# Kernel optimization log

Measured on AMD Instinct MI355X. Metric: run time of the kernel, lower is better.

## Reference

```python
import jax, jax.numpy as jnp
import numpy as np

NUM_QUANTS = 256
RES_CH = 120
SKIP_CH = 240
K = 2
NUM_BLOCKS = 16
CYCLE = 8
DILATIONS = [2 ** (i % CYCLE) for i in range(NUM_BLOCKS)]


def causal_conv1d(x, w, b, dilation=1):
    # x: [B, Cin, T], w: [Cout, Cin, K], left-pad for causality
    pad = (w.shape[-1] - 1) * dilation
    y = jax.lax.conv_general_dilated(
        x, w, window_strides=(1,), padding=[(pad, 0)],
        rhs_dilation=(dilation,), dimension_numbers=('NCH', 'OIH', 'NCH'))
    return y + b[None, :, None]


def setup_inputs() -> dict:
    key = jax.random.key(0)
    ks = jax.random.split(key, 16)
    B, T = 8, 16384
    s = 0.1
    inp = {
        'waveforms': jax.random.normal(ks[0], (B, T), jnp.float32),
        'W_in': jax.random.normal(ks[1], (RES_CH, 1, 1), jnp.float32) * s,
        'b_in': jnp.zeros((RES_CH,), jnp.float32),
        'Wf': jax.random.normal(ks[2], (NUM_BLOCKS, RES_CH, RES_CH, K), jnp.float32) * s,
        'bf': jnp.zeros((NUM_BLOCKS, RES_CH), jnp.float32),
        'Wg': jax.random.normal(ks[3], (NUM_BLOCKS, RES_CH, RES_CH, K), jnp.float32) * s,
        'bg': jnp.zeros((NUM_BLOCKS, RES_CH), jnp.float32),
        'Wres': jax.random.normal(ks[4], (NUM_BLOCKS, RES_CH, RES_CH, 1), jnp.float32) * s,
        'bres': jnp.zeros((NUM_BLOCKS, RES_CH), jnp.float32),
        'Wskip': jax.random.normal(ks[5], (NUM_BLOCKS, SKIP_CH, RES_CH, 1), jnp.float32) * s,
        'bskip': jnp.zeros((NUM_BLOCKS, SKIP_CH), jnp.float32),
        'W1': jax.random.normal(ks[6], (NUM_QUANTS, SKIP_CH, 1), jnp.float32) * s,
        'b1': jnp.zeros((NUM_QUANTS,), jnp.float32),
        'W2': jax.random.normal(ks[7], (NUM_QUANTS, NUM_QUANTS, 1), jnp.float32) * s,
        'b2': jnp.zeros((NUM_QUANTS,), jnp.float32),
    }
    return inp


def reference(waveforms, W_in, b_in, Wf, bf, Wg, bg, Wres, bres, Wskip, bskip, W1, b1, W2, b2):
    # input 1x1 conv: [B, T] -> [B, RES_CH, T]
    x = causal_conv1d(waveforms[:, None, :], W_in, b_in)
    skip_sum = jnp.zeros((x.shape[0], SKIP_CH, x.shape[2]), x.dtype)
    for i in range(NUM_BLOCKS):
        d = DILATIONS[i]
        f = jnp.tanh(causal_conv1d(x, Wf[i], bf[i], d))
        g = jax.nn.sigmoid(causal_conv1d(x, Wg[i], bg[i], d))
        z = f * g  # gated activation
        skip_sum = skip_sum + causal_conv1d(z, Wskip[i], bskip[i])
        x = x + causal_conv1d(z, Wres[i], bres[i])
    h = jax.nn.relu(skip_sum)
    h = jax.nn.relu(causal_conv1d(h, W1, b1))
    logits = causal_conv1d(h, W2, b2)  # [B, NUM_QUANTS, T]
    return logits
```

## Files before the change

kernel.cpp:

```cpp
#include <hip/hip_runtime.h>
#include <cstddef>

#define TT 16384
#define NBATCH 8
#define CH 128
#define RES 120
#define SKIPC 240
#define NQ 256
#define NT2 32
#define NTF 64
#define KZ 2048

typedef __attribute__((ext_vector_type(8))) short bf8;
typedef __attribute__((ext_vector_type(4))) short s4;
typedef __attribute__((ext_vector_type(4))) float f32x4;

__device__ __forceinline__ short f2bf(float f) {
  unsigned u = __builtin_bit_cast(unsigned, f);
  u += 0x7fffu + ((u >> 16) & 1u);
  return (short)(u >> 16);
}
__device__ __forceinline__ float bf2f(short s) {
  unsigned u = ((unsigned)(unsigned short)s) << 16;
  return __builtin_bit_cast(float, u);
}

__global__ void k_pack(const float* __restrict__ Wf, const float* __restrict__ Wg,
                       const float* __restrict__ Wres, const float* __restrict__ Wskip,
                       const float* __restrict__ W1, const float* __restrict__ W2,
                       const float* __restrict__ bf, const float* __restrict__ bg,
                       const float* __restrict__ bres, const float* __restrict__ bskip,
                       short* __restrict__ Afg, short* __restrict__ Ars,
                       short* __restrict__ W1p, short* __restrict__ W2p,
                       float* __restrict__ biasp,
                       short* __restrict__ Wskp, float* __restrict__ bsum, int do2) {
  const int NAFG = 16 * 256 * 256;
  const int NARS = 16 * 384 * 128;
  const int NW = 256 * 256;
  const int NBIA = 16 * (128 * 3 + 256);
  const int NWSK = 256 * 2048;
  const int total = NAFG + NARS + 2 * NW + NBIA + NWSK + 256;
  for (int idx = blockIdx.x * blockDim.x + threadIdx.x; idx < total;
       idx += gridDim.x * blockDim.x) {
    if (idx < NAFG) {
      int i = idx >> 16, rem = idx & 65535, m = rem >> 8, k = rem & 255;
      int tap = k >> 7, ci = k & 127;
      float v = 0.f;
      if (ci < 120) {
        if (m < 120) v = Wf[((i * 120 + m) * 120 + ci) * 2 + tap];
        else if (m >= 128 && m < 248) v = Wg[((i * 120 + (m - 128)) * 120 + ci) * 2 + tap];
      }
      Afg[idx] = f2bf(v);
    } else if (idx < NAFG + NARS) {
      int j = idx - NAFG;
      int i = j / 49152, rem = j % 49152, m = rem >> 7, k = rem & 127;
      float v = 0.f;
      if (k < 120) {
        if (m < 120) v = Wres[(i * 120 + m) * 120 + k];
        else if (m >= 128 && m < 368) v = Wskip[(i * 240 + (m - 128)) * 120 + k];
      }
      Ars[j] = f2bf(v);
    } else if (idx < NAFG + NARS + NW) {
      int j = idx - NAFG - NARS, q = j >> 8, k = j & 255;
      W1p[j] = f2bf(k < 240 ? W1[q * 240 + k] : 0.f);
    } else if (idx < NAFG + NARS + 2 * NW) {
      int j = idx - NAFG - NARS - NW;
      W2p[j] = f2bf(W2[j]);
    } else if (idx < NAFG + NARS + 2 * NW + NBIA) {
      int j = idx - NAFG - NARS - 2 * NW;
      float v = 0.f;
      if (j < 2048) { int i = j >> 7, c = j & 127; if (c < 120) v = bf[i * 120 + c]; }
      else if (j < 4096) { int jj = j - 2048; int i = jj >> 7, c = jj & 127; if (c < 120) v = bg[i * 120 + c]; }
      else if (j < 6144) { int jj = j - 4096; int i = jj >> 7, c = jj & 127; if (c < 120) v = bres[i * 120 + c]; }
      else { int jj = j - 6144; int i = jj >> 8, c = jj & 255; if (c < 240) v = bskip[i * 240 + c]; }
      biasp[j] = v;
    } else if (idx < NAFG + NARS + 2 * NW + NBIA + NWSK) {
      if (do2) {
        int j = idx - NAFG - NARS - 2 * NW - NBIA;
        int m = j >> 11, k = j & 2047;
        int layer = k >> 7, ci = k & 127;
        float v = 0.f;
        if (m < 240 && ci < 120) v = Wskip[((size_t)layer * 240 + m) * 120 + ci];
        Wskp[j] = f2bf(v);
      }
    } else {
      if (do2) {
        int m = idx - (NAFG + NARS + 2 * NW + NBIA + NWSK);
        float v = 0.f;
        if (m < 240)
          for (int l = 0; l < 16; l++) v += bskip[l * 240 + m];
        bsum[m] = v;
      }
    }
  }
}

__global__ void k_input(const float* __restrict__ wave, const float* __restrict__ win,
                        const float* __restrict__ bin, short* __restrict__ x0) {
  int idx = blockIdx.x * blockDim.x + threadIdx.x;
  if (idx >= NBATCH * TT) return;
  float wv = wave[idx];
  short* row = x0 + (size_t)idx * CH;
  for (int c = 0; c < CH; c += 4) {
    s4 v;
#pragma unroll
    for (int j = 0; j < 4; j++)
      v[j] = (c + j < 120) ? f2bf(win[c + j] * wv + bin[c + j]) : (short)0;
    *(s4*)(row + c) = v;
  }
}

__global__ __launch_bounds__(256) void k_res2(
    const short* __restrict__ xin, short* __restrict__ xout,
    short* __restrict__ zg,
    const short* __restrict__ Afg, const short* __restrict__ Ars,
    const float* __restrict__ biasp, int layer, int dil, int b_off) {
  __shared__ short xc[NT2][136];
  __shared__ short xd[NT2][136];
  __shared__ short zT[NT2][136];
  const int bl = blockIdx.y;
  const int b = b_off + bl;
  const int t0 = blockIdx.x * NT2;
  const int tid = threadIdx.x;
  const int lane = tid & 63, w = tid >> 6;
  const int l15 = lane & 15, l4 = lane >> 4;
  const size_t xbase = (size_t)b * TT * CH;

#pragma unroll
  for (int j = 0; j < 2; j++) {
    int i = tid + j * 256;
    int t = i >> 4, c8 = i & 15;
    *(bf8*)&xc[t][c8 * 8] = *(const bf8*)(xin + xbase + (size_t)(t0 + t) * CH + c8 * 8);
    int ts = t0 + t - dil;
    bf8 vd = (bf8)(short)0;
    if (ts >= 0) vd = *(const bf8*)(xin + xbase + (size_t)ts * CH + c8 * 8);
    *(bf8*)&xd[t][c8 * 8] = vd;
  }
  __syncthreads();

  f32x4 fa[2][2], ga[2][2];
#pragma unroll
  for (int i = 0; i < 2; i++)
#pragma unroll
    for (int j = 0; j < 2; j++) { fa[i][j] = (f32x4)0.f; ga[i][j] = (f32x4)0.f; }
  const short* pAf[2];
  const short* pAg[2];
#pragma unroll
  for (int mt = 0; mt < 2; mt++) {
    pAf[mt] = Afg + (size_t)(w * 32 + mt * 16 + l15) * 256 + l4 * 8;
    pAg[mt] = Afg + (size_t)(128 + w * 32 + mt * 16 + l15) * 256 + l4 * 8;
  }
#pragma unroll
  for (int kk = 0; kk < 8; kk++) {
    const int k = kk * 32;
    bf8 Bv[2];
#pragma unroll
    for (int nt = 0; nt < 2; nt++)
      Bv[nt] = (kk < 4) ? *(const bf8*)&xd[nt * 16 + l15][k + l4 * 8]
                        : *(const bf8*)&xc[nt * 16 + l15][(k - 128) + l4 * 8];
#pragma unroll
    for (int mt = 0; mt < 2; mt++) {
      bf8 Av = *(const bf8*)(pAf[mt] + k);
      bf8 Gv = *(const bf8*)(pAg[mt] + k);
#pragma unroll
      for (int nt = 0; nt < 2; nt++) {
        fa[mt][nt] = __builtin_amdgcn_mfma_f32_16x16x32_bf16(Av, Bv[nt], fa[mt][nt], 0, 0, 0);
        ga[mt][nt] = __builtin_amdgcn_mfma_f32_16x16x32_bf16(Gv, Bv[nt], ga[mt][nt], 0, 0, 0);
      }
    }
  }

  const float* bf_ = biasp + (size_t)layer * 128;
  const float* bg_ = biasp + 2048 + (size_t)layer * 128;
#pragma unroll
  for (int mt = 0; mt < 2; mt++) {
    const int mb = w * 32 + mt * 16 + l4 * 4;
#pragma unroll
    for (int nt = 0; nt < 2; nt++) {
      s4 zp;
#pragma unroll
      for (int r = 0; r < 4; r++) {
        float f = fa[mt][nt][r] + bf_[mb + r];
        float g = ga[mt][nt][r] + bg_[mb + r];
        float th = 1.f - 2.f / (__expf(2.f * f) + 1.f);
        float sg = 1.f / (1.f + __expf(-g));
        zp[r] = f2bf(th * sg);
      }
      *(s4*)&zT[nt * 16 + l15][mb] = zp;
    }
  }
  __syncthreads();

#pragma unroll
  for (int j = 0; j < 2; j++) {
    int i = tid + j * 256;
    int t = i >> 4, c8 = i & 15;
    bf8 v = *(const bf8*)&zT[t][c8 * 8];
    __builtin_nontemporal_store(
        v, (bf8*)(zg + ((size_t)(bl * TT + t0 + t) * 16 + layer) * 128 + c8 * 8));
  }

  f32x4 acc[2][2];
#pragma unroll
  for (int i = 0; i < 2; i++)
#pragma unroll
    for (int j = 0; j < 2; j++) acc[i][j] = (f32x4)0.f;
  const short* pA[2];
#pragma unroll
  for (int mt = 0; mt < 2; mt++)
    pA[mt] = Ars + (size_t)(w * 32 + mt * 16 + l15) * 128 + l4 * 8;
#pragma unroll
  for (int kk = 0; kk < 4; kk++) {
    const int k = kk * 32;
    bf8 Bv[2];
#pragma unroll
    for (int nt = 0; nt < 2; nt++) Bv[nt] = *(const bf8*)&zT[nt * 16 + l15][k + l4 * 8];
#pragma unroll
    for (int mt = 0; mt < 2; mt++) {
      bf8 Av = *(const bf8*)(pA[mt] + k);
#pragma unroll
      for (int nt = 0; nt < 2; nt++)
        acc[mt][nt] = __builtin_amdgcn_mfma_f32_16x16x32_bf16(Av, Bv[nt], acc[mt][nt], 0, 0, 0);
    }
  }

  const float* br_ = biasp + 4096 + (size_t)layer * 128;
#pragma unroll
  for (int mt = 0; mt < 2; mt++) {
    const int m = w * 32 + mt * 16 + l4 * 4;
#pragma unroll
    for (int nt = 0; nt < 2; nt++) {
      int t = t0 + nt * 16 + l15;
      s4 xv = *(const s4*)&xc[nt * 16 + l15][m];
      s4 ov;
#pragma unroll
      for (int r = 0; r < 4; r++)
        ov[r] = f2bf(bf2f(xv[r]) + acc[mt][nt][r] + br_[m + r]);
      *(s4*)(xout + xbase + (size_t)t * CH + m) = ov;
    }
  }
}

__global__ __launch_bounds__(256) void k_head2(
    const short* __restrict__ zg, const short* __restrict__ Wskp,
    const float* __restrict__ bsum,
    const short* __restrict__ W1p, const float* __restrict__ b1,
    const short* __restrict__ W2p, const float* __restrict__ b2,
    float* __restrict__ out, int b_off) {
  __shared__ short bufA[NT2][264];
  __shared__ short bufB[NT2][264];
  const int bl = blockIdx.y;
  const int b = b_off + bl;
  const int t0 = blockIdx.x * NT2;
  const int tid = threadIdx.x;
  const int lane = tid & 63, w = tid >> 6;
  const int l15 = lane & 15, l4 = lane >> 4;

  f32x4 acc[4][2];
#pragma unroll
  for (int i = 0; i < 4; i++)
#pragma unroll
    for (int j = 0; j < 2; j++) acc[i][j] = (f32x4)0.f;

  const short* zrow = zg + (size_t)(bl * TT + t0) * KZ;

#pragma unroll
  for (int j = 0; j < 4; j++) {
    int i = tid + j * 256;
    int t = i >> 5, c8 = i & 31;
    *(bf8*)&bufA[t][c8 * 8] = *(const bf8*)(zrow + (size_t)t * KZ + c8 * 8);
  }
  __syncthreads();
  for (int c = 0; c < 8; c++) {
    short (*cur)[264] = (c & 1) ? bufB : bufA;
    short (*nxt)[264] = (c & 1) ? bufA : bufB;
    if (c < 7) {
#pragma unroll
      for (int j = 0; j < 4; j++) {
        int i = tid + j * 256;
        int t = i >> 5, c8 = i & 31;
        *(bf8*)&nxt[t][c8 * 8] =
            *(const bf8*)(zrow + (size_t)t * KZ + (c + 1) * 256 + c8 * 8);
      }
    }
#pragma unroll
    for (int kk = 0; kk < 8; kk++) {
      const int k = kk * 32;
      bf8 Bv[2];
#pragma unroll
      for (int nt = 0; nt < 2; nt++)
        Bv[nt] = *(const bf8*)&cur[nt * 16 + l15][k + l4 * 8];
#pragma unroll
      for (int mt = 0; mt < 4; mt++) {
        bf8 Av = *(const bf8*)(Wskp + (size_t)(w * 64 + mt * 16 + l15) * KZ +
                               c * 256 + k + l4 * 8);
#pragma unroll
        for (int nt = 0; nt < 2; nt++)
          acc[mt][nt] = __builtin_amdgcn_mfma_f32_16x16x32_bf16(Av, Bv[nt], acc[mt][nt], 0, 0, 0);
      }
    }
    __syncthreads();
  }

#pragma unroll
  for (int mt = 0; mt < 4; mt++) {
    const int mb = w * 64 + mt * 16 + l4 * 4;
#pragma unroll
    for (int nt = 0; nt < 2; nt++) {
      s4 hp;
#pragma unroll
      for (int r = 0; r < 4; r++)
        hp[r] = f2bf(fmaxf(acc[mt][nt][r] + bsum[mb + r], 0.f));
      *(s4*)&bufA[nt * 16 + l15][mb] = hp;
    }
  }
  __syncthreads();

#pragma unroll
  for (int i = 0; i < 4; i++)
#pragma unroll
    for (int j = 0; j < 2; j++) acc[i][j] = (f32x4)0.f;
#pragma unroll
  for (int kk = 0; kk < 8; kk++) {
    const int k = kk * 32;
    bf8 Bv[2];
#pragma unroll
    for (int nt = 0; nt < 2; nt++) Bv[nt] = *(const bf8*)&bufA[nt * 16 + l15][k + l4 * 8];
#pragma unroll
    for (int mt = 0; mt < 4; mt++) {
      bf8 Av = *(const bf8*)(W1p + (size_t)(w * 64 + mt * 16 + l15) * 256 + k + l4 * 8);
#pragma unroll
      for (int nt = 0; nt < 2; nt++)
        acc[mt][nt] = __builtin_amdgcn_mfma_f32_16x16x32_bf16(Av, Bv[nt], acc[mt][nt], 0, 0, 0);
    }
  }
#pragma unroll
  for (int mt = 0; mt < 4; mt++) {
    const int mb = w * 64 + mt * 16 + l4 * 4;
#pragma unroll
    for (int nt = 0; nt < 2; nt++) {
      s4 hp;
#pragma unroll
      for (int r = 0; r < 4; r++)
        hp[r] = f2bf(fmaxf(acc[mt][nt][r] + b1[mb + r], 0.f));
      *(s4*)&bufB[nt * 16 + l15][mb] = hp;
    }
  }
  __syncthreads();

#pragma unroll
  for (int i = 0; i < 4; i++)
#pragma unroll
    for (int j = 0; j < 2; j++) acc[i][j] = (f32x4)0.f;
#pragma unroll
  for (int kk = 0; kk < 8; kk++) {
    const int k = kk * 32;
    bf8 Bv[2];
#pragma unroll
    for (int nt = 0; nt < 2; nt++) Bv[nt] = *(const bf8*)&bufB[nt * 16 + l15][k + l4 * 8];
#pragma unroll
    for (int mt = 0; mt < 4; mt++) {
      bf8 Av = *(const bf8*)(W2p + (size_t)(w * 64 + mt * 16 + l15) * 256 + k + l4 * 8);
#pragma unroll
      for (int nt = 0; nt < 2; nt++)
        acc[mt][nt] = __builtin_amdgcn_mfma_f32_16x16x32_bf16(Av, Bv[nt], acc[mt][nt], 0, 0, 0);
    }
  }
#pragma unroll
  for (int mt = 0; mt < 4; mt++) {
    const int q = w * 64 + mt * 16 + l4 * 4;
#pragma unroll
    for (int nt = 0; nt < 2; nt++) {
      int t = t0 + nt * 16 + l15;
#pragma unroll
      for (int r = 0; r < 4; r++) {
        float v = acc[mt][nt][r] + b2[q + r];
        __builtin_nontemporal_store(v, out + ((size_t)b * NQ + q + r) * TT + t);
      }
    }
  }
}

__global__ __launch_bounds__(256) void k_res_mfma(
    const short* __restrict__ xin, short* __restrict__ xout,
    float* __restrict__ skip,
    const short* __restrict__ Afg, const short* __restrict__ Ars,
    const float* __restrict__ biasp, int layer, int dil, int first) {
  __shared__ short zT[NTF][136];
  const int b = blockIdx.y;
  const int t0 = blockIdx.x * NTF;
  const int tid = threadIdx.x;
  const int lane = tid & 63, w = tid >> 6;
  const int l15 = lane & 15, l4 = lane >> 4;
  const size_t xbase = (size_t)b * TT * CH;

  f32x4 fa[2][4], ga[2][4];
#pragma unroll
  for (int i = 0; i < 2; i++)
#pragma unroll
    for (int j = 0; j < 4; j++) { fa[i][j] = (f32x4)0.f; ga[i][j] = (f32x4)0.f; }

  const short* pBd[4];
  const short* pBc[4];
  bool vld[4];
#pragma unroll
  for (int nt = 0; nt < 4; nt++) {
    int t = t0 + nt * 16 + l15;
    int ts = t - dil;
    vld[nt] = (ts >= 0);
    pBd[nt] = xin + xbase + (size_t)(vld[nt] ? ts : 0) * CH + l4 * 8;
    pBc[nt] = xin + xbase + (size_t)t * CH + l4 * 8;
  }
  const short* pAf[2];
  const short* pAg[2];
#pragma unroll
  for (int mt = 0; mt < 2; mt++) {
    pAf[mt] = Afg + (size_t)(w * 32 + mt * 16 + l15) * 256 + l4 * 8;
    pAg[mt] = Afg + (size_t)(128 + w * 32 + mt * 16 + l15) * 256 + l4 * 8;
  }
  const bf8 zv = (bf8)(short)0;
#pragma unroll
  for (int kk = 0; kk < 8; kk++) {
    const int k = kk * 32;
    bf8 Bv[4];
#pragma unroll
    for (int nt = 0; nt < 4; nt++) {
      if (kk < 4) {
        bf8 v = *(const bf8*)(pBd[nt] + k);
        Bv[nt] = vld[nt] ? v : zv;
      } else {
        Bv[nt] = *(const bf8*)(pBc[nt] + (k - 128));
      }
    }
#pragma unroll
    for (int mt = 0; mt < 2; mt++) {
      bf8 Av = *(const bf8*)(pAf[mt] + k);
      bf8 Gv = *(const bf8*)(pAg[mt] + k);
#pragma unroll
      for (int nt = 0; nt < 4; nt++) {
        fa[mt][nt] = __builtin_amdgcn_mfma_f32_16x16x32_bf16(Av, Bv[nt], fa[mt][nt], 0, 0, 0);
        ga[mt][nt] = __builtin_amdgcn_mfma_f32_16x16x32_bf16(Gv, Bv[nt], ga[mt][nt], 0, 0, 0);
      }
    }
  }

  const float* bf_ = biasp + (size_t)layer * 128;
  const float* bg_ = biasp + 2048 + (size_t)layer * 128;
#pragma unroll
  for (int mt = 0; mt < 2; mt++) {
    int mb = w * 32 + mt * 16 + l4 * 4;
#pragma unroll
    for (int nt = 0; nt < 4; nt++) {
      s4 zp;
#pragma unroll
      for (int r = 0; r < 4; r++) {
        float f = fa[mt][nt][r] + bf_[mb + r];
        float g = ga[mt][nt][r] + bg_[mb + r];
        float th = 1.f - 2.f / (__expf(2.f * f) + 1.f);
        float sg = 1.f / (1.f + __expf(-g));
        zp[r] = f2bf(th * sg);
      }
      *(s4*)&zT[nt * 16 + l15][mb] = zp;
    }
  }
  __syncthreads();

  f32x4 acc[6][4];
#pragma unroll
  for (int i = 0; i < 6; i++)
#pragma unroll
    for (int j = 0; j < 4; j++) acc[i][j] = (f32x4)0.f;
  const short* pA[6];
#pragma unroll
  for (int mt = 0; mt < 6; mt++)
    pA[mt] = Ars + (size_t)(w * 96 + mt * 16 + l15) * 128 + l4 * 8;
#pragma unroll
  for (int kk = 0; kk < 4; kk++) {
    const int k = kk * 32;
    bf8 Bv[4];
#pragma unroll
    for (int nt = 0; nt < 4; nt++) Bv[nt] = *(const bf8*)&zT[nt * 16 + l15][k + l4 * 8];
#pragma unroll
    for (int mt = 0; mt < 6; mt++) {
      bf8 Av = *(const bf8*)(pA[mt] + k);
#pragma unroll
      for (int nt = 0; nt < 4; nt++)
        acc[mt][nt] = __builtin_amdgcn_mfma_f32_16x16x32_bf16(Av, Bv[nt], acc[mt][nt], 0, 0, 0);
    }
  }

  const float* br_ = biasp + 4096 + (size_t)layer * 128;
  const float* bs_ = biasp + 6144 + (size_t)layer * 256;
#pragma unroll
  for (int mt = 0; mt < 6; mt++) {
    int m = w * 96 + mt * 16 + l4 * 4;
#pragma unroll
    for (int nt = 0; nt < 4; nt++) {
      int t = t0 + nt * 16 + l15;
      if (m < 128) {
        s4 xv = *(const s4*)(xin + xbase + (size_t)t * CH + m);
        s4 ov;
#pragma unroll
        for (int r = 0; r < 4; r++)
          ov[r] = f2bf(bf2f(xv[r]) + acc[mt][nt][r] + br_[m + r]);
        *(s4*)(xout + xbase + (size_t)t * CH + m) = ov;
      } else if (m < 128 + SKIPC) {
        int c = m - 128;
        float* sp = skip + ((size_t)b * NQ + c) * TT + t;
#pragma unroll
        for (int r = 0; r < 4; r++) {
          float v = acc[mt][nt][r] + bs_[c + r];
          if (!first) v += sp[(size_t)r * TT];
          sp[(size_t)r * TT] = v;
        }
      }
    }
  }
}

__global__ __launch_bounds__(256) void k_head_mfma(
    const float* skip, const short* __restrict__ W1p, const float* __restrict__ b1,
    const short* __restrict__ W2p, const float* __restrict__ b2, float* out) {
  __shared__ short hT[NTF][264];
  __shared__ short h2T[NTF][264];
  const int b = blockIdx.y;
  const int t0 = blockIdx.x * NTF;
  const int tid = threadIdx.x;
  const int lane = tid & 63, w = tid >> 6;
  const int l15 = lane & 15, l4 = lane >> 4;

  for (int u = tid; u < 256 * 16; u += 256) {
    int c = u >> 4, tq = u & 15;
    if (c < SKIPC) {
      f32x4 v = *(const f32x4*)(skip + ((size_t)b * NQ + c) * TT + t0 + tq * 4);
#pragma unroll
      for (int j = 0; j < 4; j++) hT[tq * 4 + j][c] = f2bf(fmaxf(v[j], 0.f));
    } else {
#pragma unroll
      for (int j = 0; j < 4; j++) hT[tq * 4 + j][c] = 0;
    }
  }
  __syncthreads();

  f32x4 acc[4][4];
#pragma unroll
  for (int i = 0; i < 4; i++)
#pragma unroll
    for (int j = 0; j < 4; j++) acc[i][j] = (f32x4)0.f;
#pragma unroll
  for (int kk = 0; kk < 8; kk++) {
    const int k = kk * 32;
    bf8 Bv[4];
#pragma unroll
    for (int nt = 0; nt < 4; nt++) Bv[nt] = *(const bf8*)&hT[nt * 16 + l15][k + l4 * 8];
#pragma unroll
    for (int mt = 0; mt < 4; mt++) {
      bf8 Av = *(const bf8*)(W1p + (size_t)(w * 64 + mt * 16 + l15) * 256 + k + l4 * 8);
#pragma unroll
      for (int nt = 0; nt < 4; nt++)
        acc[mt][nt] = __builtin_amdgcn_mfma_f32_16x16x32_bf16(Av, Bv[nt], acc[mt][nt], 0, 0, 0);
    }
  }
#pragma unroll
  for (int mt = 0; mt < 4; mt++) {
    int mb = w * 64 + mt * 16 + l4 * 4;
#pragma unroll
    for (int nt = 0; nt < 4; nt++) {
      s4 hp;
#pragma unroll
      for (int r = 0; r < 4; r++) hp[r] = f2bf(fmaxf(acc[mt][nt][r] + b1[mb + r], 0.f));
      *(s4*)&h2T[nt * 16 + l15][mb] = hp;
    }
  }
  __syncthreads();

#pragma unroll
  for (int i = 0; i < 4; i++)
#pragma unroll
    for (int j = 0; j < 4; j++) acc[i][j] = (f32x4)0.f;
#pragma unroll
  for (int kk = 0; kk < 8; kk++) {
    const int k = kk * 32;
    bf8 Bv[4];
#pragma unroll
    for (int nt = 0; nt < 4; nt++) Bv[nt] = *(const bf8*)&h2T[nt * 16 + l15][k + l4 * 8];
#pragma unroll
    for (int mt = 0; mt < 4; mt++) {
      bf8 Av = *(const bf8*)(W2p + (size_t)(w * 64 + mt * 16 + l15) * 256 + k + l4 * 8);
#pragma unroll
      for (int nt = 0; nt < 4; nt++)
        acc[mt][nt] = __builtin_amdgcn_mfma_f32_16x16x32_bf16(Av, Bv[nt], acc[mt][nt], 0, 0, 0);
    }
  }
#pragma unroll
  for (int mt = 0; mt < 4; mt++) {
    int q = w * 64 + mt * 16 + l4 * 4;
#pragma unroll
    for (int nt = 0; nt < 4; nt++) {
      int t = t0 + nt * 16 + l15;
#pragma unroll
      for (int r = 0; r < 4; r++)
        out[((size_t)b * NQ + q + r) * TT + t] = acc[mt][nt][r] + b2[q + r];
    }
  }
}

extern "C" void kernel_launch(void* const* d_in, const int* in_sizes, int n_in,
                              void* d_out, int out_size, void* d_ws, size_t ws_size,
                              hipStream_t stream) {
  const float* wave  = (const float*)d_in[0];
  const float* W_in  = (const float*)d_in[1];
  const float* b_in  = (const float*)d_in[2];
  const float* Wf    = (const float*)d_in[3];
  const float* bf    = (const float*)d_in[4];
  const float* Wg    = (const float*)d_in[5];
  const float* bg    = (const float*)d_in[6];
  const float* Wres  = (const float*)d_in[7];
  const float* bres  = (const float*)d_in[8];
  const float* Wskip = (const float*)d_in[9];
  const float* bskip = (const float*)d_in[10];
  const float* W1    = (const float*)d_in[11];
  const float* b1    = (const float*)d_in[12];
  const float* W2    = (const float*)d_in[13];
  const float* b2    = (const float*)d_in[14];
  float* out = (float*)d_out;

  char* ws = (char*)d_ws;
  short* xA    = (short*)ws;
  short* xB    = (short*)(ws + 33554432);
  short* Afg   = (short*)(ws + 67108864);
  short* Ars   = (short*)(ws + 69206016);
  short* W1p   = (short*)(ws + 70778880);
  short* W2p   = (short*)(ws + 70909952);
  float* biasp = (float*)(ws + 71041024);
  short* Wskp  = (short*)(ws + 71081984);
  float* bsum  = (float*)(ws + 72130560);
  short* zg    = (short*)(ws + 72131584);
  const size_t BASE = 72131584ull;
  const size_t ZPB  = (size_t)TT * KZ * 2;

  int nbg = 0;
  if      (ws_size >= BASE + 8 * ZPB) nbg = 8;
  else if (ws_size >= BASE + 4 * ZPB) nbg = 4;
  else if (ws_size >= BASE + 2 * ZPB) nbg = 2;
  else if (ws_size >= BASE + 1 * ZPB) nbg = 1;

  k_pack<<<1024, 256, 0, stream>>>(Wf, Wg, Wres, Wskip, W1, W2, bf, bg, bres, bskip,
                                   Afg, Ars, W1p, W2p, biasp, Wskp, bsum,
                                   nbg > 0 ? 1 : 0);
  k_input<<<(NBATCH * TT) / 256, 256, 0, stream>>>(wave, W_in, b_in, xA);

  static const int dils[16] = {1, 2, 4, 8, 16, 32, 64, 128,
                               1, 2, 4, 8, 16, 32, 64, 128};
  if (nbg > 0) {
    for (int g = 0; g < NBATCH; g += nbg) {
      const short* xi = xA;
      short* xo = xB;
      for (int i = 0; i < 16; i++) {
        k_res2<<<dim3(TT / NT2, nbg), 256, 0, stream>>>(
            xi, xo, zg, Afg + (size_t)i * 65536, Ars + (size_t)i * 49152,
            biasp, i, dils[i], g);
        short* tmp = (short*)xi; xi = xo; xo = tmp;
      }
      k_head2<<<dim3(TT / NT2, nbg), 256, 0, stream>>>(zg, Wskp, bsum, W1p, b1,
                                                       W2p, b2, out, g);
    }
  } else {
    const short* xi = xA;
    short* xo = xB;
    for (int i = 0; i < 16; i++) {
      k_res_mfma<<<dim3(TT / NTF, NBATCH), 256, 0, stream>>>(
          xi, xo, out, Afg + (size_t)i * 65536, Ars + (size_t)i * 49152,
          biasp, i, dils[i], i == 0 ? 1 : 0);
      short* tmp = (short*)xi; xi = xo; xo = tmp;
    }
    k_head_mfma<<<dim3(TT / NTF, NBATCH), 256, 0, stream>>>(out, W1p, b1, W2p, b2, out);
  }
}
```

Before: 2.500 ms.

## Split fused head into tiled skip GEMM and separate 1x1 head kernel

Replaces the fused head kernel, which streamed the Wskp weights from global memory for every 32-timestep tile, with a dedicated 128x128-tiled skip GEMM kernel. That kernel stages both operands in double-buffered LDS and writes relu(skip) in fp32 into the output buffer. A second kernel, launched once after all batch groups, reads those fp32 values back, converts them to bf16 and applies the two 256-wide 1x1 convs with 64-timestep tiles. Batch grouping also now uses any workspace size up to 8 and handles a partial last group. The aim is better weight reuse and MFMA density in the K=2048 skip GEMM, at the cost of an extra fp32 round trip through the output buffer.

```diff
diff --git a/kernel.cpp b/kernel.cpp
--- a/kernel.cpp
+++ b/kernel.cpp
@@ -241,109 +241,135 @@
   }
 }
 
-__global__ __launch_bounds__(256) void k_head2(
+__global__ __launch_bounds__(256) void k_skip(
     const short* __restrict__ zg, const short* __restrict__ Wskp,
-    const float* __restrict__ bsum,
-    const short* __restrict__ W1p, const float* __restrict__ b1,
-    const short* __restrict__ W2p, const float* __restrict__ b2,
-    float* __restrict__ out, int b_off) {
-  __shared__ short bufA[NT2][264];
-  __shared__ short bufB[NT2][264];
-  const int bl = blockIdx.y;
+    const float* __restrict__ bsum, float* __restrict__ out, int b_off) {
+  __shared__ short At[2][128][40];
+  __shared__ short Bt[2][128][40];
+  const int tid = threadIdx.x;
+  const int lane = tid & 63;
+  const int w = tid >> 6;
+  const int wm = w >> 1, wn = w & 1;
+  const int l15 = lane & 15, l4 = lane >> 4;
+
+  const int m0 = blockIdx.y * 128;
+  const int bl = blockIdx.x >> 7;
+  const int t0 = (blockIdx.x & 127) << 7;
   const int b = b_off + bl;
-  const int t0 = blockIdx.x * NT2;
+
+  const short* Asrc = Wskp + (size_t)m0 * KZ;
+  const short* Bsrc = zg + ((size_t)bl * TT + t0) * KZ;
+
+  const int sr = tid >> 1;
+  const int sc = (tid & 1) * 16;
+
+  f32x4 acc[4][4];
+#pragma unroll
+  for (int i = 0; i < 4; i++)
+#pragma unroll
+    for (int j = 0; j < 4; j++) acc[i][j] = (f32x4)0.f;
+
+  bf8 ra0, ra1, rb0, rb1;
+  ra0 = *(const bf8*)(Asrc + (size_t)sr * KZ + sc);
+  ra1 = *(const bf8*)(Asrc + (size_t)sr * KZ + sc + 8);
+  rb0 = *(const bf8*)(Bsrc + (size_t)sr * KZ + sc);
+  rb1 = *(const bf8*)(Bsrc + (size_t)sr * KZ + sc + 8);
+  *(bf8*)&At[0][sr][sc] = ra0; *(bf8*)&At[0][sr][sc + 8] = ra1;
+  *(bf8*)&Bt[0][sr][sc] = rb0; *(bf8*)&Bt[0][sr][sc + 8] = rb1;
+  __syncthreads();
+
+  for (int ks = 0; ks < 64; ks++) {
+    const int cur = ks & 1;
+    if (ks < 63) {
+      const int k1 = (ks + 1) * 32;
+      ra0 = *(const bf8*)(Asrc + (size_t)sr * KZ + k1 + sc);
+      ra1 = *(const bf8*)(Asrc + (size_t)sr * KZ + k1 + sc + 8);
+      rb0 = *(const bf8*)(Bsrc + (size_t)sr * KZ + k1 + sc);
+      rb1 = *(const bf8*)(Bsrc + (size_t)sr * KZ + k1 + sc + 8);
+    }
+    bf8 Af[4], Bf[4];
+#pragma unroll
+    for (int mt = 0; mt < 4; mt++)
+      Af[mt] = *(const bf8*)&At[cur][wm * 64 + mt * 16 + l15][l4 * 8];
+#pragma unroll
+    for (int nt = 0; nt < 4; nt++)
+      Bf[nt] = *(const bf8*)&Bt[cur][wn * 64 + nt * 16 + l15][l4 * 8];
+#pragma unroll
+    for (int mt = 0; mt < 4; mt++)
+#pragma unroll
+      for (int nt = 0; nt < 4; nt++)
+        acc[mt][nt] = __builtin_amdgcn_mfma_f32_16x16x32_bf16(Af[mt], Bf[nt], acc[mt][nt], 0, 0, 0);
+    if (ks < 63) {
+      __syncthreads();
+      *(bf8*)&At[cur ^ 1][sr][sc] = ra0; *(bf8*)&At[cur ^ 1][sr][sc + 8] = ra1;
+      *(bf8*)&Bt[cur ^ 1][sr][sc] = rb0; *(bf8*)&Bt[cur ^ 1][sr][sc + 8] = rb1;
+      __syncthreads();
+    }
+  }
+
+#pragma unroll
+  for (int mt = 0; mt < 4; mt++) {
+    const int m = m0 + wm * 64 + mt * 16 + l4 * 4;
+#pragma unroll
+    for (int nt = 0; nt < 4; nt++) {
+      const int t = t0 + wn * 64 + nt * 16 + l15;
+#pragma unroll
+      for (int r = 0; r < 4; r++) {
+        float h = fmaxf(acc[mt][nt][r] + bsum[m + r], 0.f);
+        out[((size_t)b * NQ + m + r) * TT + t] = h;
+      }
+    }
+  }
+}
+
+__global__ __launch_bounds__(256) void k_headW(
+    float* out, const short* __restrict__ W1p, const float* __restrict__ b1,
+    const short* __restrict__ W2p, const float* __restrict__ b2) {
+  __shared__ short hT[NTF][264];
+  __shared__ short h2T[NTF][264];
+  const int b = blockIdx.y;
+  const int t0 = blockIdx.x * NTF;
   const int tid = threadIdx.x;
   const int lane = tid & 63, w = tid >> 6;
   const int l15 = lane & 15, l4 = lane >> 4;
-
-  f32x4 acc[4][2];
+  const float* hb = out + (size_t)b * NQ * TT;
+
+#pragma unroll 4
+  for (int p = 0; p < 64; p++) {
+    int c = p * 4 + (tid >> 6);
+    float v = hb[(size_t)c * TT + t0 + lane];
+    hT[lane][c] = f2bf(v);
+  }
+  __syncthreads();
+
+  f32x4 acc[4][4];
 #pragma unroll
   for (int i = 0; i < 4; i++)
 #pragma unroll
-    for (int j = 0; j < 2; j++) acc[i][j] = (f32x4)0.f;
-
-  const short* zrow = zg + (size_t)(bl * TT + t0) * KZ;
-
-#pragma unroll
-  for (int j = 0; j < 4; j++) {
-    int i = tid + j * 256;
-    int t = i >> 5, c8 = i & 31;
-    *(bf8*)&bufA[t][c8 * 8] = *(const bf8*)(zrow + (size_t)t * KZ + c8 * 8);
-  }
-  __syncthreads();
-  for (int c = 0; c < 8; c++) {
-    short (*cur)[264] = (c & 1) ? bufB : bufA;
-    short (*nxt)[264] = (c & 1) ? bufA : bufB;
-    if (c < 7) {
-#pragma unroll
-      for (int j = 0; j < 4; j++) {
-        int i = tid + j * 256;
-        int t = i >> 5, c8 = i & 31;
-        *(bf8*)&nxt[t][c8 * 8] =
-            *(const bf8*)(zrow + (size_t)t * KZ + (c + 1) * 256 + c8 * 8);
-      }
-    }
-#pragma unroll
-    for (int kk = 0; kk < 8; kk++) {
-      const int k = kk * 32;
-      bf8 Bv[2];
-#pragma unroll
-      for (int nt = 0; nt < 2; nt++)
-        Bv[nt] = *(const bf8*)&cur[nt * 16 + l15][k + l4 * 8];
-#pragma unroll
-      for (int mt = 0; mt < 4; mt++) {
-        bf8 Av = *(const bf8*)(Wskp + (size_t)(w * 64 + mt * 16 + l15) * KZ +
-                               c * 256 + k + l4 * 8);
-#pragma unroll
-        for (int nt = 0; nt < 2; nt++)
-          acc[mt][nt] = __builtin_amdgcn_mfma_f32_16x16x32_bf16(Av, Bv[nt], acc[mt][nt], 0, 0, 0);
-      }
-    }
-    __syncthreads();
-  }
-
-#pragma unroll
-  for (int mt = 0; mt < 4; mt++) {
-    const int mb = w * 64 + mt * 16 + l4 * 4;
-#pragma unroll
-    for (int nt = 0; nt < 2; nt++) {
-      s4 hp;
-#pragma unroll
-      for (int r = 0; r < 4; r++)
-        hp[r] = f2bf(fmaxf(acc[mt][nt][r] + bsum[mb + r], 0.f));
-      *(s4*)&bufA[nt * 16 + l15][mb] = hp;
-    }
-  }
-  __syncthreads();
-
-#pragma unroll
-  for (int i = 0; i < 4; i++)
-#pragma unroll
-    for (int j = 0; j < 2; j++) acc[i][j] = (f32x4)0.f;
+    for (int j = 0; j < 4; j++) acc[i][j] = (f32x4)0.f;
 #pragma unroll
   for (int kk = 0; kk < 8; kk++) {
     const int k = kk * 32;
-    bf8 Bv[2];
-#pragma unroll
-    for (int nt = 0; nt < 2; nt++) Bv[nt] = *(const bf8*)&bufA[nt * 16 + l15][k + l4 * 8];
+    bf8 Bv[4];
+#pragma unroll
+    for (int nt = 0; nt < 4; nt++) Bv[nt] = *(const bf8*)&hT[nt * 16 + l15][k + l4 * 8];
 #pragma unroll
     for (int mt = 0; mt < 4; mt++) {
       bf8 Av = *(const bf8*)(W1p + (size_t)(w * 64 + mt * 16 + l15) * 256 + k + l4 * 8);
 #pragma unroll
-      for (int nt = 0; nt < 2; nt++)
+      for (int nt = 0; nt < 4; nt++)
         acc[mt][nt] = __builtin_amdgcn_mfma_f32_16x16x32_bf16(Av, Bv[nt], acc[mt][nt], 0, 0, 0);
     }
   }
 #pragma unroll
   for (int mt = 0; mt < 4; mt++) {
-    const int mb = w * 64 + mt * 16 + l4 * 4;
-#pragma unroll
-    for (int nt = 0; nt < 2; nt++) {
+    int mb = w * 64 + mt * 16 + l4 * 4;
+#pragma unroll
+    for (int nt = 0; nt < 4; nt++) {
       s4 hp;
 #pragma unroll
-      for (int r = 0; r < 4; r++)
-        hp[r] = f2bf(fmaxf(acc[mt][nt][r] + b1[mb + r], 0.f));
-      *(s4*)&bufB[nt * 16 + l15][mb] = hp;
+      for (int r = 0; r < 4; r++) hp[r] = f2bf(fmaxf(acc[mt][nt][r] + b1[mb + r], 0.f));
+      *(s4*)&h2T[nt * 16 + l15][mb] = hp;
     }
   }
   __syncthreads();
@@ -351,32 +377,30 @@
 #pragma unroll
   for (int i = 0; i < 4; i++)
 #pragma unroll
-    for (int j = 0; j < 2; j++) acc[i][j] = (f32x4)0.f;
+    for (int j = 0; j < 4; j++) acc[i][j] = (f32x4)0.f;
 #pragma unroll
   for (int kk = 0; kk < 8; kk++) {
     const int k = kk * 32;
-    bf8 Bv[2];
-#pragma unroll
-    for (int nt = 0; nt < 2; nt++) Bv[nt] = *(const bf8*)&bufB[nt * 16 + l15][k + l4 * 8];
+    bf8 Bv[4];
+#pragma unroll
+    for (int nt = 0; nt < 4; nt++) Bv[nt] = *(const bf8*)&h2T[nt * 16 + l15][k + l4 * 8];
 #pragma unroll
     for (int mt = 0; mt < 4; mt++) {
       bf8 Av = *(const bf8*)(W2p + (size_t)(w * 64 + mt * 16 + l15) * 256 + k + l4 * 8);
 #pragma unroll
-      for (int nt = 0; nt < 2; nt++)
+      for (int nt = 0; nt < 4; nt++)
         acc[mt][nt] = __builtin_amdgcn_mfma_f32_16x16x32_bf16(Av, Bv[nt], acc[mt][nt], 0, 0, 0);
     }
   }
 #pragma unroll
   for (int mt = 0; mt < 4; mt++) {
-    const int q = w * 64 + mt * 16 + l4 * 4;
-#pragma unroll
-    for (int nt = 0; nt < 2; nt++) {
+    int q = w * 64 + mt * 16 + l4 * 4;
+#pragma unroll
+    for (int nt = 0; nt < 4; nt++) {
       int t = t0 + nt * 16 + l15;
 #pragma unroll
-      for (int r = 0; r < 4; r++) {
-        float v = acc[mt][nt][r] + b2[q + r];
-        __builtin_nontemporal_store(v, out + ((size_t)b * NQ + q + r) * TT + t);
-      }
+      for (int r = 0; r < 4; r++)
+        out[((size_t)b * NQ + q + r) * TT + t] = acc[mt][nt][r] + b2[q + r];
     }
   }
 }
@@ -640,10 +664,10 @@
   const size_t ZPB  = (size_t)TT * KZ * 2;
 
   int nbg = 0;
-  if      (ws_size >= BASE + 8 * ZPB) nbg = 8;
-  else if (ws_size >= BASE + 4 * ZPB) nbg = 4;
-  else if (ws_size >= BASE + 2 * ZPB) nbg = 2;
-  else if (ws_size >= BASE + 1 * ZPB) nbg = 1;
+  if (ws_size > BASE) {
+    size_t k = (ws_size - BASE) / ZPB;
+    nbg = (int)(k > 8 ? 8 : k);
+  }
 
   k_pack<<<1024, 256, 0, stream>>>(Wf, Wg, Wres, Wskip, W1, W2, bf, bg, bres, bskip,
                                    Afg, Ars, W1p, W2p, biasp, Wskp, bsum,
@@ -654,17 +678,18 @@
                                1, 2, 4, 8, 16, 32, 64, 128};
   if (nbg > 0) {
     for (int g = 0; g < NBATCH; g += nbg) {
+      const int rem = (NBATCH - g) < nbg ? (NBATCH - g) : nbg;
       const short* xi = xA;
       short* xo = xB;
       for (int i = 0; i < 16; i++) {
-        k_res2<<<dim3(TT / NT2, nbg), 256, 0, stream>>>(
+        k_res2<<<dim3(TT / NT2, rem), 256, 0, stream>>>(
             xi, xo, zg, Afg + (size_t)i * 65536, Ars + (size_t)i * 49152,
             biasp, i, dils[i], g);
         short* tmp = (short*)xi; xi = xo; xo = tmp;
       }
-      k_head2<<<dim3(TT / NT2, nbg), 256, 0, stream>>>(zg, Wskp, bsum, W1p, b1,
-                                                       W2p, b2, out, g);
-    }
+      k_skip<<<dim3(rem * (TT / 128), 2), 256, 0, stream>>>(zg, Wskp, bsum, out, g);
+    }
+    k_headW<<<dim3(TT / NTF, NBATCH), 256, 0, stream>>>(out, W1p, b1, W2p, b2);
   } else {
     const short* xi = xA;
     short* xo = xB;
```

Result: faster. 2.139 ms (-14.5%).
